# Kernel tuning notes

Measured on AMD Instinct MI355X. Metric: run time of the kernel, lower is better.

The kernel has to match this reference:

```python
import jax, jax.numpy as jnp
import numpy as np
from jax import lax

MAX_DISP = 10  # init kwarg max_displacement
EPS = 1e-12    # torch F.normalize default eps


def _l2_normalize(x, axis):
    # matches torch.nn.functional.normalize: x / max(||x||_2, eps)
    norm = jnp.sqrt(jnp.sum(x * x, axis=axis, keepdims=True))
    return x / jnp.maximum(norm, EPS)


def setup_inputs() -> dict:
    key = jax.random.key(0)
    k1, k2 = jax.random.split(key)
    B, C, T = 8, 1024, 4096
    feat1 = jax.random.normal(k1, (B, C, T), dtype=jnp.float32)
    feat2 = jax.random.normal(k2, (B, C, T), dtype=jnp.float32)
    return {"feat1": feat1, "feat2": feat2}


def reference(feat1, feat2):
    B, C, T = feat1.shape
    f1 = _l2_normalize(feat1, axis=1)
    f2 = _l2_normalize(feat2, axis=1)
    # replicate-pad along time: [B, C, T + 2*MAX_DISP]
    f2p = jnp.pad(f2, ((0, 0), (0, 0), (MAX_DISP, MAX_DISP)), mode="edge")
    # 2*MAX_DISP+1 sliding dot-products over the channel dim; small fixed
    # offset loop (21 iters), each a fused multiply+channel-reduce -> [B, T]
    corrs = [
        jnp.sum(f1 * lax.dynamic_slice_in_dim(f2p, o, T, axis=2), axis=1)
        for o in range(2 * MAX_DISP + 1)
    ]
    return jnp.stack(corrs, axis=1)  # [B, 2*MAX_DISP+1, T]
```

## Files before the change

kernel.cpp:

```cpp
#include <hip/hip_runtime.h>


constexpr int B  = 8;
constexpr int C  = 1024;
constexpr int T  = 4096;
constexpr int NO = 21;
constexpr int MD = 10;

typedef __attribute__((ext_vector_type(8))) short short8;
typedef __attribute__((ext_vector_type(4))) float f32x4;

__device__ inline unsigned bf16rne(float f) {
    unsigned u = __float_as_uint(f);
    return (u + 0x7FFFu + ((u >> 16) & 1u)) >> 16;
}
__device__ inline unsigned pack2(float lo, float hi) {
    return bf16rne(lo) | (bf16rne(hi) << 16);
}

struct Regs { float4 a0, a1, b0, b0b, b1, b1b; };

__global__ __launch_bounds__(256)
void corr_mfma(const float* __restrict__ f1, const float* __restrict__ f2,
               float* __restrict__ out)
{
    __shared__ short8 stgv[2][640];
    __shared__ float  sq1buf[64][17];
    __shared__ float  sq2buf[4][96];
    __shared__ float  inv1L[64];
    __shared__ float  inv2L[96];
    __shared__ float  outT[NO][68];

    const int sb   = (int)blockIdx.x;
    const int flat = (sb & 7) * 64 + (sb >> 3);
    const int b    = flat >> 6;
    const int t0   = (flat & 63) * 64;

    const int tid  = (int)threadIdx.x;
    const int lane = tid & 63;
    const int w    = tid >> 6;

    const int u1 = tid & 15;
    const int q1 = tid >> 4;
    const int r2 = tid & 15;
    const int q2 = tid >> 4;
    const bool x2 = (r2 < 8);

    const float* f1p = f1 + ((size_t)b * C + 2 * q1) * T + t0 + 4 * u1;
    const float* f2p = f2 + ((size_t)b * C + 2 * q2) * T;
    const int cA = min(max(t0 - 16 + 4 * r2,        0), T - 4);
    const int cB = min(max(t0 - 16 + 4 * (16 + r2), 0), T - 4);

    const int f1hw = (u1 >> 2) * 512 + 4 * (u1 & 3) * 32
                   + ((((q1 >> 2) + (u1 & 3)) & 3) << 3) + 2 * (q1 & 3);
    const int f2hwA = 2048 + (r2 >> 2) * 512 + 4 * (r2 & 3) * 32
                    + ((((q2 >> 2) + (r2 & 3)) & 3) << 3) + 2 * (q2 & 3);
    const int f2hwB = f2hwA + 2048;

    const int ft  = lane & 15;
    const int fhw = ft * 32 + ((((lane >> 4) + (ft >> 2)) & 3) << 3);

    float sq1[4]  = {0.f, 0.f, 0.f, 0.f};
    float sq2a[4] = {0.f, 0.f, 0.f, 0.f};
    float sq2b[4] = {0.f, 0.f, 0.f, 0.f};
    f32x4 acc0 = {0.f,0.f,0.f,0.f}, acc1 = {0.f,0.f,0.f,0.f}, acc2 = {0.f,0.f,0.f,0.f};

    auto load_chunk = [&](int k) {
        Regs r; const size_t o = (size_t)k * 32 * T;
        r.a0  = *(const float4*)(f1p + o);
        r.a1  = *(const float4*)(f1p + o + T);
        r.b0  = *(const float4*)(f2p + o + cA);
        r.b0b = *(const float4*)(f2p + o + cA + T);
        if (x2) {
            r.b1  = *(const float4*)(f2p + o + cB);
            r.b1b = *(const float4*)(f2p + o + cB + T);
        }
        return r;
    };
    auto commit = [&](const Regs& r, int buf) {
        unsigned short* S = (unsigned short*)&stgv[buf][0];
        const float* a0 = (const float*)&r.a0;  const float* a1 = (const float*)&r.a1;
        const float* b0 = (const float*)&r.b0;  const float* b0b = (const float*)&r.b0b;
        const float* b1 = (const float*)&r.b1;  const float* b1b = (const float*)&r.b1b;
#pragma unroll
        for (int i = 0; i < 4; ++i) {
            *(unsigned*)&S[f1hw  + 32 * i] = pack2(a0[i], a1[i]);
            *(unsigned*)&S[f2hwA + 32 * i] = pack2(b0[i], b0b[i]);
            sq1[i]  += a0[i] * a0[i] + a1[i] * a1[i];
            sq2a[i] += b0[i] * b0[i] + b0b[i] * b0b[i];
        }
        if (x2) {
#pragma unroll
            for (int i = 0; i < 4; ++i) {
                *(unsigned*)&S[f2hwB + 32 * i] = pack2(b1[i], b1b[i]);
                sq2b[i] += b1[i] * b1[i] + b1b[i] * b1b[i];
            }
        }
    };
    auto compute = [&](int buf) {
        const unsigned short* S = (const unsigned short*)&stgv[buf][0];
        short8 af  = *(const short8*)&S[w * 512 + fhw];
        short8 bf0 = *(const short8*)&S[2048 + (w + 0) * 512 + fhw];
        short8 bf1 = *(const short8*)&S[2048 + (w + 1) * 512 + fhw];
        short8 bf2 = *(const short8*)&S[2048 + (w + 2) * 512 + fhw];
        acc0 = __builtin_amdgcn_mfma_f32_16x16x32_bf16(af, bf0, acc0, 0, 0, 0);
        acc1 = __builtin_amdgcn_mfma_f32_16x16x32_bf16(af, bf1, acc1, 0, 0, 0);
        acc2 = __builtin_amdgcn_mfma_f32_16x16x32_bf16(af, bf2, acc2, 0, 0, 0);
    };

    Regs RA = load_chunk(0), RB = load_chunk(1);
    for (int k = 0; k < 32; k += 2) {
        commit(RA, 0);
        __syncthreads();
        if (k + 2 < 32) RA = load_chunk(k + 2);
        compute(0);
        commit(RB, 1);
        __syncthreads();
        if (k + 3 < 32) RB = load_chunk(k + 3);
        compute(1);
    }

#pragma unroll
    for (int e = 0; e < 4; ++e) sq1buf[4 * u1 + e][q1] = sq1[e];
#pragma unroll
    for (int i = 0; i < 4; ++i) {
        sq2a[i] += __shfl_xor(sq2a[i], 16, 64);
        sq2a[i] += __shfl_xor(sq2a[i], 32, 64);
        sq2b[i] += __shfl_xor(sq2b[i], 16, 64);
        sq2b[i] += __shfl_xor(sq2b[i], 32, 64);
    }
    if (lane < 16) {
#pragma unroll
        for (int i = 0; i < 4; ++i) sq2buf[w][4 * lane + i] = sq2a[i];
    }
    if (lane < 8) {
#pragma unroll
        for (int i = 0; i < 4; ++i) sq2buf[w][64 + 4 * lane + i] = sq2b[i];
    }
    __syncthreads();
    if (tid < 64) {
        float s = 0.f;
#pragma unroll
        for (int g = 0; g < 16; ++g) s += sq1buf[tid][g];
        inv1L[tid] = 1.f / fmaxf(sqrtf(s), 1e-12f);
    } else if (tid < 160) {
        const int f = tid - 64;
        float s = sq2buf[0][f] + sq2buf[1][f] + sq2buf[2][f] + sq2buf[3][f];
        inv2L[f] = 1.f / fmaxf(sqrtf(s), 1e-12f);
    }
    __syncthreads();

    const int m0  = t0 + w * 16;
    const int cr  = lane & 15;
    const int rr4 = (lane >> 4) * 4;
#define EPI(nt, A)                                                          \
    {                                                                       \
        const int tp = t0 - 16 + (w + (nt)) * 16 + cr;                      \
        _Pragma("unroll")                                                   \
        for (int r = 0; r < 4; ++r) {                                       \
            const int t = m0 + rr4 + r;                                     \
            const int d = tp - t;                                           \
            if (tp >= 0 && tp < T && d >= -MD && d <= MD) {                 \
                const float val = (A)[r] * inv1L[t - t0] * inv2L[tp - t0 + 16]; \
                const int on  = d + MD;                                     \
                const int olo = (tp == 0)     ? 0      : on;                \
                const int ohi = (tp == T - 1) ? NO - 1 : on;                \
                for (int o = olo; o <= ohi; ++o) outT[o][t - t0] = val;     \
            }                                                               \
        }                                                                   \
    }
    EPI(0, acc0) EPI(1, acc1) EPI(2, acc2)
#undef EPI
    __syncthreads();

    for (int task = tid; task < NO * 16; task += 256) {
        const int o  = task >> 4;
        const int t4 = (task & 15) * 4;
        const float4 v = *(const float4*)&outT[o][t4];
        *(float4*)(out + ((size_t)b * NO + o) * T + t0 + t4) = v;
    }
}

extern "C" void kernel_launch(void* const* d_in, const int* in_sizes, int n_in,
                              void* d_out, int out_size, void* d_ws, size_t ws_size,
                              hipStream_t stream)
{
    const float* f1 = (const float*)d_in[0];
    const float* f2 = (const float*)d_in[1];
    (void)d_ws; (void)ws_size;
    corr_mfma<<<dim3(512), dim3(256), 0, stream>>>(f1, f2, (float*)d_out);
}
```

Measured before the change: 45.82 us.

## Split channel reduction across two wave groups per block and merge accumulators

Doubles the block to 512 threads and splits the 1024-channel reduction into two halves, each handled by four waves with its own double-buffered LDS staging. The second half's MFMA accumulators are merged into the first half through shared memory before the epilogue. The LDS layout also changes to a padded row stride, which alters bank mapping for fragment loads. The goal is more memory-level parallelism and a shorter serial chunk loop per block, at the cost of more LDS, an extra merge step and lower occupancy per CU.

```diff
diff --git a/kernel.cpp b/kernel.cpp
--- a/kernel.cpp
+++ b/kernel.cpp
@@ -1,11 +1,15 @@
 #include <hip/hip_runtime.h>
 
 
-constexpr int B  = 8;
-constexpr int C  = 1024;
-constexpr int T  = 4096;
-constexpr int NO = 21;
-constexpr int MD = 10;
+constexpr int B    = 8;
+constexpr int C    = 1024;
+constexpr int T    = 4096;
+constexpr int NO   = 21;
+constexpr int MD   = 10;
+constexpr int CH   = 512;
+constexpr int NCHK = 16;
+constexpr int TSTR = 520;
+constexpr int HBUF = 5200;
 
 typedef __attribute__((ext_vector_type(8))) short short8;
 typedef __attribute__((ext_vector_type(4))) float f32x4;
@@ -20,13 +24,13 @@
 
 struct Regs { float4 a0, a1, b0, b0b, b1, b1b; };
 
-__global__ __launch_bounds__(256)
+__global__ __launch_bounds__(512)
 void corr_mfma(const float* __restrict__ f1, const float* __restrict__ f2,
                float* __restrict__ out)
 {
-    __shared__ short8 stgv[2][640];
-    __shared__ float  sq1buf[64][17];
-    __shared__ float  sq2buf[4][96];
+    __shared__ short8 stgv[4][650];
+    __shared__ float  sq1buf[64][33];
+    __shared__ float  sq2buf[8][96];
     __shared__ float  inv1L[64];
     __shared__ float  inv2L[96];
     __shared__ float  outT[NO][68];
@@ -39,26 +43,28 @@
     const int tid  = (int)threadIdx.x;
     const int lane = tid & 63;
     const int w    = tid >> 6;
-
-    const int u1 = tid & 15;
-    const int q1 = tid >> 4;
-    const int r2 = tid & 15;
-    const int q2 = tid >> 4;
+    const int wm   = w & 3;
+    const int h    = w >> 2;
+    const int ht   = tid & 255;
+
+    const int u1 = ht & 15;
+    const int q1 = ht >> 4;
+    const int r2 = ht & 15;
+    const int q2 = ht >> 4;
     const bool x2 = (r2 < 8);
 
-    const float* f1p = f1 + ((size_t)b * C + 2 * q1) * T + t0 + 4 * u1;
-    const float* f2p = f2 + ((size_t)b * C + 2 * q2) * T;
+    const float* f1p = f1 + ((size_t)(b * C + h * CH + 2 * q1)) * T + t0 + 4 * u1;
+    const float* f2p = f2 + ((size_t)(b * C + h * CH + 2 * q2)) * T;
     const int cA = min(max(t0 - 16 + 4 * r2,        0), T - 4);
     const int cB = min(max(t0 - 16 + 4 * (16 + r2), 0), T - 4);
 
-    const int f1hw = (u1 >> 2) * 512 + 4 * (u1 & 3) * 32
-                   + ((((q1 >> 2) + (u1 & 3)) & 3) << 3) + 2 * (q1 & 3);
-    const int f2hwA = 2048 + (r2 >> 2) * 512 + 4 * (r2 & 3) * 32
-                    + ((((q2 >> 2) + (r2 & 3)) & 3) << 3) + 2 * (q2 & 3);
-    const int f2hwB = f2hwA + 2048;
-
-    const int ft  = lane & 15;
-    const int fhw = ft * 32 + ((((lane >> 4) + (ft >> 2)) & 3) << 3);
+    const int f1hw  = (u1 >> 2) * TSTR + ((q1 >> 2) * 16 + 4 * (u1 & 3)) * 8 + 2 * (q1 & 3);
+    const int f2hwA = 4 * TSTR + (r2 >> 2) * TSTR
+                    + ((q2 >> 2) * 16 + 4 * (r2 & 3)) * 8 + 2 * (q2 & 3);
+    const int f2hwB = f2hwA + 4 * TSTR;
+
+    const int fhwA  = wm * TSTR + lane * 8;
+    const int fhwB0 = 4 * TSTR + wm * TSTR + lane * 8;
 
     float sq1[4]  = {0.f, 0.f, 0.f, 0.f};
     float sq2a[4] = {0.f, 0.f, 0.f, 0.f};
@@ -78,50 +84,50 @@
         return r;
     };
     auto commit = [&](const Regs& r, int buf) {
-        unsigned short* S = (unsigned short*)&stgv[buf][0];
-        const float* a0 = (const float*)&r.a0;  const float* a1 = (const float*)&r.a1;
+        unsigned short* S = (unsigned short*)&stgv[h * 2 + buf][0];
+        const float* a0 = (const float*)&r.a0;  const float* a1  = (const float*)&r.a1;
         const float* b0 = (const float*)&r.b0;  const float* b0b = (const float*)&r.b0b;
         const float* b1 = (const float*)&r.b1;  const float* b1b = (const float*)&r.b1b;
 #pragma unroll
         for (int i = 0; i < 4; ++i) {
-            *(unsigned*)&S[f1hw  + 32 * i] = pack2(a0[i], a1[i]);
-            *(unsigned*)&S[f2hwA + 32 * i] = pack2(b0[i], b0b[i]);
+            *(unsigned*)&S[f1hw  + 8 * i] = pack2(a0[i], a1[i]);
+            *(unsigned*)&S[f2hwA + 8 * i] = pack2(b0[i], b0b[i]);
             sq1[i]  += a0[i] * a0[i] + a1[i] * a1[i];
             sq2a[i] += b0[i] * b0[i] + b0b[i] * b0b[i];
         }
         if (x2) {
 #pragma unroll
             for (int i = 0; i < 4; ++i) {
-                *(unsigned*)&S[f2hwB + 32 * i] = pack2(b1[i], b1b[i]);
+                *(unsigned*)&S[f2hwB + 8 * i] = pack2(b1[i], b1b[i]);
                 sq2b[i] += b1[i] * b1[i] + b1b[i] * b1b[i];
             }
         }
     };
     auto compute = [&](int buf) {
-        const unsigned short* S = (const unsigned short*)&stgv[buf][0];
-        short8 af  = *(const short8*)&S[w * 512 + fhw];
-        short8 bf0 = *(const short8*)&S[2048 + (w + 0) * 512 + fhw];
-        short8 bf1 = *(const short8*)&S[2048 + (w + 1) * 512 + fhw];
-        short8 bf2 = *(const short8*)&S[2048 + (w + 2) * 512 + fhw];
+        const unsigned short* S = (const unsigned short*)&stgv[h * 2 + buf][0];
+        short8 af  = *(const short8*)&S[fhwA];
+        short8 bf0 = *(const short8*)&S[fhwB0];
+        short8 bf1 = *(const short8*)&S[fhwB0 + TSTR];
+        short8 bf2 = *(const short8*)&S[fhwB0 + 2 * TSTR];
         acc0 = __builtin_amdgcn_mfma_f32_16x16x32_bf16(af, bf0, acc0, 0, 0, 0);
         acc1 = __builtin_amdgcn_mfma_f32_16x16x32_bf16(af, bf1, acc1, 0, 0, 0);
         acc2 = __builtin_amdgcn_mfma_f32_16x16x32_bf16(af, bf2, acc2, 0, 0, 0);
     };
 
     Regs RA = load_chunk(0), RB = load_chunk(1);
-    for (int k = 0; k < 32; k += 2) {
+    for (int k = 0; k < NCHK; k += 2) {
         commit(RA, 0);
         __syncthreads();
-        if (k + 2 < 32) RA = load_chunk(k + 2);
+        if (k + 2 < NCHK) RA = load_chunk(k + 2);
         compute(0);
         commit(RB, 1);
         __syncthreads();
-        if (k + 3 < 32) RB = load_chunk(k + 3);
+        if (k + 3 < NCHK) RB = load_chunk(k + 3);
         compute(1);
     }
 
 #pragma unroll
-    for (int e = 0; e < 4; ++e) sq1buf[4 * u1 + e][q1] = sq1[e];
+    for (int e = 0; e < 4; ++e) sq1buf[4 * u1 + e][q1 + 16 * h] = sq1[e];
 #pragma unroll
     for (int i = 0; i < 4; ++i) {
         sq2a[i] += __shfl_xor(sq2a[i], 16, 64);
@@ -138,42 +144,57 @@
         for (int i = 0; i < 4; ++i) sq2buf[w][64 + 4 * lane + i] = sq2b[i];
     }
     __syncthreads();
+
+    f32x4* mrg = (f32x4*)&stgv[0][0];
+    if (h == 1) {
+        const int mb = (wm * 64 + lane) * 3;
+        mrg[mb + 0] = acc0; mrg[mb + 1] = acc1; mrg[mb + 2] = acc2;
+    }
     if (tid < 64) {
         float s = 0.f;
 #pragma unroll
-        for (int g = 0; g < 16; ++g) s += sq1buf[tid][g];
+        for (int g = 0; g < 32; ++g) s += sq1buf[tid][g];
         inv1L[tid] = 1.f / fmaxf(sqrtf(s), 1e-12f);
     } else if (tid < 160) {
         const int f = tid - 64;
-        float s = sq2buf[0][f] + sq2buf[1][f] + sq2buf[2][f] + sq2buf[3][f];
+        float s = 0.f;
+#pragma unroll
+        for (int g = 0; g < 8; ++g) s += sq2buf[g][f];
         inv2L[f] = 1.f / fmaxf(sqrtf(s), 1e-12f);
     }
     __syncthreads();
 
-    const int m0  = t0 + w * 16;
-    const int cr  = lane & 15;
-    const int rr4 = (lane >> 4) * 4;
+    if (h == 0) {
+        const int mb = (wm * 64 + lane) * 3;
+        f32x4 m0v = mrg[mb + 0], m1v = mrg[mb + 1], m2v = mrg[mb + 2];
+#pragma unroll
+        for (int r = 0; r < 4; ++r) { acc0[r] += m0v[r]; acc1[r] += m1v[r]; acc2[r] += m2v[r]; }
+
+        const int m0  = t0 + wm * 16;
+        const int cr  = lane & 15;
+        const int rr4 = (lane >> 4) * 4;
 #define EPI(nt, A)                                                          \
-    {                                                                       \
-        const int tp = t0 - 16 + (w + (nt)) * 16 + cr;                      \
-        _Pragma("unroll")                                                   \
-        for (int r = 0; r < 4; ++r) {                                       \
-            const int t = m0 + rr4 + r;                                     \
-            const int d = tp - t;                                           \
-            if (tp >= 0 && tp < T && d >= -MD && d <= MD) {                 \
-                const float val = (A)[r] * inv1L[t - t0] * inv2L[tp - t0 + 16]; \
-                const int on  = d + MD;                                     \
-                const int olo = (tp == 0)     ? 0      : on;                \
-                const int ohi = (tp == T - 1) ? NO - 1 : on;                \
-                for (int o = olo; o <= ohi; ++o) outT[o][t - t0] = val;     \
+        {                                                                   \
+            const int tp = t0 - 16 + (wm + (nt)) * 16 + cr;                 \
+            _Pragma("unroll")                                               \
+            for (int r = 0; r < 4; ++r) {                                   \
+                const int t = m0 + rr4 + r;                                 \
+                const int d = tp - t;                                       \
+                if (tp >= 0 && tp < T && d >= -MD && d <= MD) {             \
+                    const float val = (A)[r] * inv1L[t - t0] * inv2L[tp - t0 + 16]; \
+                    const int on  = d + MD;                                 \
+                    const int olo = (tp == 0)     ? 0      : on;            \
+                    const int ohi = (tp == T - 1) ? NO - 1 : on;            \
+                    for (int o = olo; o <= ohi; ++o) outT[o][t - t0] = val; \
+                }                                                           \
             }                                                               \
-        }                                                                   \
-    }
-    EPI(0, acc0) EPI(1, acc1) EPI(2, acc2)
+        }
+        EPI(0, acc0) EPI(1, acc1) EPI(2, acc2)
 #undef EPI
+    }
     __syncthreads();
 
-    for (int task = tid; task < NO * 16; task += 256) {
+    for (int task = tid; task < NO * 16; task += 512) {
         const int o  = task >> 4;
         const int t4 = (task & 15) * 4;
         const float4 v = *(const float4*)&outT[o][t4];
@@ -188,5 +209,5 @@
     const float* f1 = (const float*)d_in[0];
     const float* f2 = (const float*)d_in[1];
     (void)d_ws; (void)ws_size;
-    corr_mfma<<<dim3(512), dim3(256), 0, stream>>>(f1, f2, (float*)d_out);
-}
+    corr_mfma<<<dim3(512), dim3(512), 0, stream>>>(f1, f2, (float*)d_out);
+}
```

New measurement: 66.59 us. 45.3% more time.

## Split channel reduction four ways and add a finalize kernel for normalization

Applied to the files above, without the earlier changes.

The main MFMA kernel now runs on a 3D grid that splits the 1024-channel reduction into 4 slices. This gives four times as many blocks, which should fill the GPU better and keep more memory requests in flight. Each slice writes raw partial dot products and partial squared norms to workspace. A second kernel sums the partials, applies the inverse L2 norms and handles the edge-replicated offsets. The cost is extra workspace traffic, a second kernel launch, and a shorter per-block pipeline of only 8 chunks.

```diff
diff --git a/kernel.cpp b/kernel.cpp
--- a/kernel.cpp
+++ b/kernel.cpp
@@ -1,11 +1,14 @@
 #include <hip/hip_runtime.h>
 
 
-constexpr int B  = 8;
-constexpr int C  = 1024;
-constexpr int T  = 4096;
-constexpr int NO = 21;
-constexpr int MD = 10;
+constexpr int B   = 8;
+constexpr int C   = 1024;
+constexpr int T   = 4096;
+constexpr int NO  = 21;
+constexpr int MD  = 10;
+constexpr int CS  = 4;
+constexpr int CPS = C / CS;
+constexpr int NCHK = CPS / 32;
 
 typedef __attribute__((ext_vector_type(8))) short short8;
 typedef __attribute__((ext_vector_type(4))) float f32x4;
@@ -22,19 +25,19 @@
 
 __global__ __launch_bounds__(256)
 void corr_mfma(const float* __restrict__ f1, const float* __restrict__ f2,
-               float* __restrict__ out)
+               float* __restrict__ dots, float* __restrict__ s1p,
+               float* __restrict__ s2p)
 {
     __shared__ short8 stgv[2][640];
     __shared__ float  sq1buf[64][17];
     __shared__ float  sq2buf[4][96];
-    __shared__ float  inv1L[64];
-    __shared__ float  inv2L[96];
     __shared__ float  outT[NO][68];
 
-    const int sb   = (int)blockIdx.x;
-    const int flat = (sb & 7) * 64 + (sb >> 3);
-    const int b    = flat >> 6;
-    const int t0   = (flat & 63) * 64;
+    const int sx   = (int)blockIdx.x;
+    const int tile = (sx & 7) * 8 + (sx >> 3);
+    const int b    = (int)blockIdx.y;
+    const int cs   = (int)blockIdx.z;
+    const int t0   = tile * 64;
 
     const int tid  = (int)threadIdx.x;
     const int lane = tid & 63;
@@ -46,8 +49,8 @@
     const int q2 = tid >> 4;
     const bool x2 = (r2 < 8);
 
-    const float* f1p = f1 + ((size_t)b * C + 2 * q1) * T + t0 + 4 * u1;
-    const float* f2p = f2 + ((size_t)b * C + 2 * q2) * T;
+    const float* f1p = f1 + ((size_t)b * C + cs * CPS + 2 * q1) * T + t0 + 4 * u1;
+    const float* f2p = f2 + ((size_t)b * C + cs * CPS + 2 * q2) * T;
     const int cA = min(max(t0 - 16 + 4 * r2,        0), T - 4);
     const int cB = min(max(t0 - 16 + 4 * (16 + r2), 0), T - 4);
 
@@ -79,7 +82,7 @@
     };
     auto commit = [&](const Regs& r, int buf) {
         unsigned short* S = (unsigned short*)&stgv[buf][0];
-        const float* a0 = (const float*)&r.a0;  const float* a1 = (const float*)&r.a1;
+        const float* a0 = (const float*)&r.a0;  const float* a1  = (const float*)&r.a1;
         const float* b0 = (const float*)&r.b0;  const float* b0b = (const float*)&r.b0b;
         const float* b1 = (const float*)&r.b1;  const float* b1b = (const float*)&r.b1b;
 #pragma unroll
@@ -109,14 +112,14 @@
     };
 
     Regs RA = load_chunk(0), RB = load_chunk(1);
-    for (int k = 0; k < 32; k += 2) {
+    for (int k = 0; k < NCHK; k += 2) {
         commit(RA, 0);
         __syncthreads();
-        if (k + 2 < 32) RA = load_chunk(k + 2);
+        if (k + 2 < NCHK) RA = load_chunk(k + 2);
         compute(0);
         commit(RB, 1);
         __syncthreads();
-        if (k + 3 < 32) RB = load_chunk(k + 3);
+        if (k + 3 < NCHK) RB = load_chunk(k + 3);
         compute(1);
     }
 
@@ -142,13 +145,13 @@
         float s = 0.f;
 #pragma unroll
         for (int g = 0; g < 16; ++g) s += sq1buf[tid][g];
-        inv1L[tid] = 1.f / fmaxf(sqrtf(s), 1e-12f);
+        s1p[((size_t)cs * B + b) * T + t0 + tid] = s;
     } else if (tid < 160) {
         const int f = tid - 64;
         float s = sq2buf[0][f] + sq2buf[1][f] + sq2buf[2][f] + sq2buf[3][f];
-        inv2L[f] = 1.f / fmaxf(sqrtf(s), 1e-12f);
-    }
-    __syncthreads();
+        if (f >= 16 && f < 80)
+            s2p[((size_t)cs * B + b) * T + t0 + f - 16] = s;
+    }
 
     const int m0  = t0 + w * 16;
     const int cr  = lane & 15;
@@ -160,13 +163,8 @@
         for (int r = 0; r < 4; ++r) {                                       \
             const int t = m0 + rr4 + r;                                     \
             const int d = tp - t;                                           \
-            if (tp >= 0 && tp < T && d >= -MD && d <= MD) {                 \
-                const float val = (A)[r] * inv1L[t - t0] * inv2L[tp - t0 + 16]; \
-                const int on  = d + MD;                                     \
-                const int olo = (tp == 0)     ? 0      : on;                \
-                const int ohi = (tp == T - 1) ? NO - 1 : on;                \
-                for (int o = olo; o <= ohi; ++o) outT[o][t - t0] = val;     \
-            }                                                               \
+            if (tp >= 0 && tp < T && d >= -MD && d <= MD)                   \
+                outT[d + MD][t - t0] = (A)[r];                              \
         }                                                                   \
     }
     EPI(0, acc0) EPI(1, acc1) EPI(2, acc2)
@@ -177,7 +175,49 @@
         const int o  = task >> 4;
         const int t4 = (task & 15) * 4;
         const float4 v = *(const float4*)&outT[o][t4];
-        *(float4*)(out + ((size_t)b * NO + o) * T + t0 + t4) = v;
+        *(float4*)(dots + (((size_t)cs * B + b) * NO + o) * T + t0 + t4) = v;
+    }
+}
+
+__global__ __launch_bounds__(256)
+void corr_fin(const float* __restrict__ dots, const float* __restrict__ s1p,
+              const float* __restrict__ s2p, float* __restrict__ out)
+{
+    __shared__ float inv2s[276];
+    const int bx  = (int)blockIdx.x;
+    const int b   = bx >> 4;
+    const int tc  = (bx & 15) * 256;
+    const int tid = (int)threadIdx.x;
+    const int t   = tc + tid;
+
+    auto inv_of = [&](const float* p, int tt) {
+        float s = 0.f;
+#pragma unroll
+        for (int cs = 0; cs < CS; ++cs) s += p[((size_t)cs * B + b) * T + tt];
+        return 1.f / fmaxf(sqrtf(s), 1e-12f);
+    };
+
+    const float i1 = inv_of(s1p, t);
+    inv2s[10 + tid] = inv_of(s2p, t);
+    if (tid < 10) {
+        const int tl = max(tc - 10 + tid, 0);
+        inv2s[tid] = inv_of(s2p, tl);
+    }
+    if (tid >= 246) {
+        const int tr = min(tc + 256 + (tid - 246), T - 1);
+        inv2s[266 + (tid - 246)] = inv_of(s2p, tr);
+    }
+    __syncthreads();
+
+#pragma unroll
+    for (int o = 0; o < NO; ++o) {
+        const int tp = min(max(t + o - MD, 0), T - 1);
+        const int o2 = tp - t + MD;
+        float s = 0.f;
+#pragma unroll
+        for (int cs = 0; cs < CS; ++cs)
+            s += dots[(((size_t)cs * B + b) * NO + o2) * T + t];
+        out[((size_t)b * NO + o) * T + t] = s * i1 * inv2s[10 + (tp - tc)];
     }
 }
 
@@ -187,6 +227,12 @@
 {
     const float* f1 = (const float*)d_in[0];
     const float* f2 = (const float*)d_in[1];
-    (void)d_ws; (void)ws_size;
-    corr_mfma<<<dim3(512), dim3(256), 0, stream>>>(f1, f2, (float*)d_out);
-}
+    float* wsf  = (float*)d_ws;
+    float* dots = wsf;
+    float* s1p  = dots + (size_t)CS * B * NO * T;
+    float* s2p  = s1p  + (size_t)CS * B * T;
+    (void)ws_size;
+
+    corr_mfma<<<dim3(64, 8, CS), dim3(256), 0, stream>>>(f1, f2, dots, s1p, s2p);
+    corr_fin<<<dim3(128), dim3(256), 0, stream>>>(dots, s1p, s2p, (float*)d_out);
+}
```

After: 56.07 us. 1.22x slower.

## Load MFMA fragments directly from global memory, dropping the LDS staging

Applied to the files above, without the earlier changes.

Each lane now loads its bf16 MFMA operand fragments straight from global memory as scalar float loads, with 8 channels per lane at its own time index. This replaces the float4 loads, the swizzled LDS staging and the per-chunk __syncthreads. The square-norm reductions become per-lane with wave shuffles, and the hand-written bf16 rounding is swapped for the HIP intrinsic. Each wave now loads its f2 neighbourhood redundantly, about 3x, and issues scalar 4-byte loads instead of 16-byte vector loads, which raises load-instruction count and cache traffic. In exchange it removes the barriers, the LDS round-trip and the launch bound that limited occupancy.

```diff
diff --git a/kernel.cpp b/kernel.cpp
--- a/kernel.cpp
+++ b/kernel.cpp
@@ -1,4 +1,5 @@
 #include <hip/hip_runtime.h>
+#include <hip/hip_bf16.h>
 
 
 constexpr int B  = 8;
@@ -9,27 +10,22 @@
 
 typedef __attribute__((ext_vector_type(8))) short short8;
 typedef __attribute__((ext_vector_type(4))) float f32x4;
+typedef __attribute__((ext_vector_type(4))) unsigned int u32x4;
 
-__device__ inline unsigned bf16rne(float f) {
-    unsigned u = __float_as_uint(f);
-    return (u + 0x7FFFu + ((u >> 16) & 1u)) >> 16;
-}
-__device__ inline unsigned pack2(float lo, float hi) {
-    return bf16rne(lo) | (bf16rne(hi) << 16);
+__device__ inline unsigned cvt2(float lo, float hi) {
+    __hip_bfloat162 h = __float22bfloat162_rn(make_float2(lo, hi));
+    return *reinterpret_cast<unsigned*>(&h);
 }
 
-struct Regs { float4 a0, a1, b0, b0b, b1, b1b; };
+struct Frag { float a[8]; float b0[8]; float b1[8]; float b2[8]; };
 
-__global__ __launch_bounds__(256)
-void corr_mfma(const float* __restrict__ f1, const float* __restrict__ f2,
-               float* __restrict__ out)
+__global__ __launch_bounds__(256, 2)
+void corr_direct(const float* __restrict__ f1, const float* __restrict__ f2,
+                 float* __restrict__ out)
 {
-    __shared__ short8 stgv[2][640];
-    __shared__ float  sq1buf[64][17];
-    __shared__ float  sq2buf[4][96];
-    __shared__ float  inv1L[64];
-    __shared__ float  inv2L[96];
-    __shared__ float  outT[NO][68];
+    __shared__ float inv1L[64];
+    __shared__ float inv2L[96];
+    __shared__ float outT[NO][68];
 
     const int sb   = (int)blockIdx.x;
     const int flat = (sb & 7) * 64 + (sb >> 3);
@@ -39,132 +35,92 @@
     const int tid  = (int)threadIdx.x;
     const int lane = tid & 63;
     const int w    = tid >> 6;
+    const int lm   = lane & 15;
+    const int ks   = lane >> 4;
+    const int m0   = t0 + w * 16;
 
-    const int u1 = tid & 15;
-    const int q1 = tid >> 4;
-    const int r2 = tid & 15;
-    const int q2 = tid >> 4;
-    const bool x2 = (r2 < 8);
+    const float* f1b = f1 + (size_t)b * C * T + m0 + lm;
+    const float* f2b = f2 + (size_t)b * C * T;
+    int tp[3];
+#pragma unroll
+    for (int n = 0; n < 3; ++n)
+        tp[n] = min(max(t0 - 16 + 16 * (w + n) + lm, 0), T - 1);
 
-    const float* f1p = f1 + ((size_t)b * C + 2 * q1) * T + t0 + 4 * u1;
-    const float* f2p = f2 + ((size_t)b * C + 2 * q2) * T;
-    const int cA = min(max(t0 - 16 + 4 * r2,        0), T - 4);
-    const int cB = min(max(t0 - 16 + 4 * (16 + r2), 0), T - 4);
-
-    const int f1hw = (u1 >> 2) * 512 + 4 * (u1 & 3) * 32
-                   + ((((q1 >> 2) + (u1 & 3)) & 3) << 3) + 2 * (q1 & 3);
-    const int f2hwA = 2048 + (r2 >> 2) * 512 + 4 * (r2 & 3) * 32
-                    + ((((q2 >> 2) + (r2 & 3)) & 3) << 3) + 2 * (q2 & 3);
-    const int f2hwB = f2hwA + 2048;
-
-    const int ft  = lane & 15;
-    const int fhw = ft * 32 + ((((lane >> 4) + (ft >> 2)) & 3) << 3);
-
-    float sq1[4]  = {0.f, 0.f, 0.f, 0.f};
-    float sq2a[4] = {0.f, 0.f, 0.f, 0.f};
-    float sq2b[4] = {0.f, 0.f, 0.f, 0.f};
     f32x4 acc0 = {0.f,0.f,0.f,0.f}, acc1 = {0.f,0.f,0.f,0.f}, acc2 = {0.f,0.f,0.f,0.f};
+    float sq1 = 0.f, sq2 = 0.f, sq2e = 0.f;
 
     auto load_chunk = [&](int k) {
-        Regs r; const size_t o = (size_t)k * 32 * T;
-        r.a0  = *(const float4*)(f1p + o);
-        r.a1  = *(const float4*)(f1p + o + T);
-        r.b0  = *(const float4*)(f2p + o + cA);
-        r.b0b = *(const float4*)(f2p + o + cA + T);
-        if (x2) {
-            r.b1  = *(const float4*)(f2p + o + cB);
-            r.b1b = *(const float4*)(f2p + o + cB + T);
+        Frag F; const int cb = k * 32 * T;
+#pragma unroll
+        for (int j = 0; j < 8; ++j) {
+            const int co = cb + (8 * ks + j) * T;
+            F.a[j]  = f1b[co];
+            F.b0[j] = f2b[co + tp[0]];
+            F.b1[j] = f2b[co + tp[1]];
+            F.b2[j] = f2b[co + tp[2]];
         }
-        return r;
+        return F;
     };
-    auto commit = [&](const Regs& r, int buf) {
-        unsigned short* S = (unsigned short*)&stgv[buf][0];
-        const float* a0 = (const float*)&r.a0;  const float* a1 = (const float*)&r.a1;
-        const float* b0 = (const float*)&r.b0;  const float* b0b = (const float*)&r.b0b;
-        const float* b1 = (const float*)&r.b1;  const float* b1b = (const float*)&r.b1b;
+    auto process = [&](const Frag& F) {
+        u32x4 ua, u0, u1, u2;
 #pragma unroll
         for (int i = 0; i < 4; ++i) {
-            *(unsigned*)&S[f1hw  + 32 * i] = pack2(a0[i], a1[i]);
-            *(unsigned*)&S[f2hwA + 32 * i] = pack2(b0[i], b0b[i]);
-            sq1[i]  += a0[i] * a0[i] + a1[i] * a1[i];
-            sq2a[i] += b0[i] * b0[i] + b0b[i] * b0b[i];
+            ua[i] = cvt2(F.a[2*i],  F.a[2*i+1]);
+            u0[i] = cvt2(F.b0[2*i], F.b0[2*i+1]);
+            u1[i] = cvt2(F.b1[2*i], F.b1[2*i+1]);
+            u2[i] = cvt2(F.b2[2*i], F.b2[2*i+1]);
         }
-        if (x2) {
+        const short8 af = __builtin_bit_cast(short8, ua);
+        acc0 = __builtin_amdgcn_mfma_f32_16x16x32_bf16(af, __builtin_bit_cast(short8, u0), acc0, 0, 0, 0);
+        acc1 = __builtin_amdgcn_mfma_f32_16x16x32_bf16(af, __builtin_bit_cast(short8, u1), acc1, 0, 0, 0);
+        acc2 = __builtin_amdgcn_mfma_f32_16x16x32_bf16(af, __builtin_bit_cast(short8, u2), acc2, 0, 0, 0);
 #pragma unroll
-            for (int i = 0; i < 4; ++i) {
-                *(unsigned*)&S[f2hwB + 32 * i] = pack2(b1[i], b1b[i]);
-                sq2b[i] += b1[i] * b1[i] + b1b[i] * b1b[i];
-            }
+        for (int j = 0; j < 8; ++j) {
+            sq1 += F.a[j]  * F.a[j];
+            sq2 += F.b1[j] * F.b1[j];
+        }
+        if (w == 0) {
+#pragma unroll
+            for (int j = 0; j < 8; ++j) sq2e += F.b0[j] * F.b0[j];
+        } else if (w == 3) {
+#pragma unroll
+            for (int j = 0; j < 8; ++j) sq2e += F.b2[j] * F.b2[j];
         }
     };
-    auto compute = [&](int buf) {
-        const unsigned short* S = (const unsigned short*)&stgv[buf][0];
-        short8 af  = *(const short8*)&S[w * 512 + fhw];
-        short8 bf0 = *(const short8*)&S[2048 + (w + 0) * 512 + fhw];
-        short8 bf1 = *(const short8*)&S[2048 + (w + 1) * 512 + fhw];
-        short8 bf2 = *(const short8*)&S[2048 + (w + 2) * 512 + fhw];
-        acc0 = __builtin_amdgcn_mfma_f32_16x16x32_bf16(af, bf0, acc0, 0, 0, 0);
-        acc1 = __builtin_amdgcn_mfma_f32_16x16x32_bf16(af, bf1, acc1, 0, 0, 0);
-        acc2 = __builtin_amdgcn_mfma_f32_16x16x32_bf16(af, bf2, acc2, 0, 0, 0);
-    };
 
-    Regs RA = load_chunk(0), RB = load_chunk(1);
+    Frag F0 = load_chunk(0), F1 = load_chunk(1);
     for (int k = 0; k < 32; k += 2) {
-        commit(RA, 0);
-        __syncthreads();
-        if (k + 2 < 32) RA = load_chunk(k + 2);
-        compute(0);
-        commit(RB, 1);
-        __syncthreads();
-        if (k + 3 < 32) RB = load_chunk(k + 3);
-        compute(1);
+        process(F0);
+        if (k + 2 < 32) F0 = load_chunk(k + 2);
+        process(F1);
+        if (k + 3 < 32) F1 = load_chunk(k + 3);
     }
 
-#pragma unroll
-    for (int e = 0; e < 4; ++e) sq1buf[4 * u1 + e][q1] = sq1[e];
-#pragma unroll
-    for (int i = 0; i < 4; ++i) {
-        sq2a[i] += __shfl_xor(sq2a[i], 16, 64);
-        sq2a[i] += __shfl_xor(sq2a[i], 32, 64);
-        sq2b[i] += __shfl_xor(sq2b[i], 16, 64);
-        sq2b[i] += __shfl_xor(sq2b[i], 32, 64);
-    }
+    sq1  += __shfl_xor(sq1, 16, 64);  sq1  += __shfl_xor(sq1, 32, 64);
+    sq2  += __shfl_xor(sq2, 16, 64);  sq2  += __shfl_xor(sq2, 32, 64);
+    sq2e += __shfl_xor(sq2e, 16, 64); sq2e += __shfl_xor(sq2e, 32, 64);
     if (lane < 16) {
-#pragma unroll
-        for (int i = 0; i < 4; ++i) sq2buf[w][4 * lane + i] = sq2a[i];
-    }
-    if (lane < 8) {
-#pragma unroll
-        for (int i = 0; i < 4; ++i) sq2buf[w][64 + 4 * lane + i] = sq2b[i];
-    }
-    __syncthreads();
-    if (tid < 64) {
-        float s = 0.f;
-#pragma unroll
-        for (int g = 0; g < 16; ++g) s += sq1buf[tid][g];
-        inv1L[tid] = 1.f / fmaxf(sqrtf(s), 1e-12f);
-    } else if (tid < 160) {
-        const int f = tid - 64;
-        float s = sq2buf[0][f] + sq2buf[1][f] + sq2buf[2][f] + sq2buf[3][f];
-        inv2L[f] = 1.f / fmaxf(sqrtf(s), 1e-12f);
+        inv1L[w * 16 + lane]        = 1.f / fmaxf(sqrtf(sq1), 1e-12f);
+        inv2L[16 * (w + 1) + lane]  = 1.f / fmaxf(sqrtf(sq2), 1e-12f);
+        if (w == 0) inv2L[lane]      = 1.f / fmaxf(sqrtf(sq2e), 1e-12f);
+        if (w == 3) inv2L[80 + lane] = 1.f / fmaxf(sqrtf(sq2e), 1e-12f);
     }
     __syncthreads();
 
-    const int m0  = t0 + w * 16;
     const int cr  = lane & 15;
     const int rr4 = (lane >> 4) * 4;
 #define EPI(nt, A)                                                          \
     {                                                                       \
-        const int tp = t0 - 16 + (w + (nt)) * 16 + cr;                      \
+        const int tpp = t0 - 16 + (w + (nt)) * 16 + cr;                     \
         _Pragma("unroll")                                                   \
         for (int r = 0; r < 4; ++r) {                                       \
             const int t = m0 + rr4 + r;                                     \
-            const int d = tp - t;                                           \
-            if (tp >= 0 && tp < T && d >= -MD && d <= MD) {                 \
-                const float val = (A)[r] * inv1L[t - t0] * inv2L[tp - t0 + 16]; \
+            const int d = tpp - t;                                          \
+            if (tpp >= 0 && tpp < T && d >= -MD && d <= MD) {               \
+                const float val = (A)[r] * inv1L[t - t0] * inv2L[tpp - t0 + 16]; \
                 const int on  = d + MD;                                     \
-                const int olo = (tp == 0)     ? 0      : on;                \
-                const int ohi = (tp == T - 1) ? NO - 1 : on;                \
+                const int olo = (tpp == 0)     ? 0      : on;               \
+                const int ohi = (tpp == T - 1) ? NO - 1 : on;               \
                 for (int o = olo; o <= ohi; ++o) outT[o][t - t0] = val;     \
             }                                                               \
         }                                                                   \
@@ -188,5 +144,5 @@
     const float* f1 = (const float*)d_in[0];
     const float* f2 = (const float*)d_in[1];
     (void)d_ws; (void)ws_size;
-    corr_mfma<<<dim3(512), dim3(256), 0, stream>>>(f1, f2, (float*)d_out);
+    corr_direct<<<dim3(512), dim3(256), 0, stream>>>(f1, f2, (float*)d_out);
 }
```

Measured after the change: 58.84 us. 1.28x slower.
